# Kernel tuning notes

Measured on AMD Instinct MI355X. Metric: run time of the kernel, lower is better.

Reference implementation:

```python
import jax, jax.numpy as jnp
import numpy as np

ALPHA = 0.2        # LeakyReLU negative slope
NEG_BIG = -9e15    # mask fill value from the original module


def setup_inputs() -> dict:
    key = jax.random.key(0)
    k1, k2, k3, k4 = jax.random.split(key, 4)
    B, N, F_in, F_out = 4, 4096, 128, 64
    h = jax.random.normal(k1, (B, N, F_in), dtype=jnp.float32)
    adj = jax.random.randint(k2, (N, N), 0, 2, dtype=jnp.int32)
    W = jax.random.normal(k3, (F_in, F_out), dtype=jnp.float32)
    a = jax.random.normal(k4, (2 * F_out, 1), dtype=jnp.float32)
    return {"h": h, "adj": adj, "W": W, "a": a}


def reference(h, adj, W, a):
    # h: [B, N, F_in], adj: [N, N], W: [F_in, F_out], a: [2*F_out, 1]
    F_out = W.shape[1]
    hW = jnp.einsum('bni,io->bno', h, W)               # [B, N, F_out]
    f1 = hW @ a[:F_out, :]                             # [B, N, 1]
    f2 = hW @ a[F_out:, :]                             # [B, N, 1]
    e = f1 + jnp.swapaxes(f2, 1, 2)                    # [B, N, N] broadcast-add
    e = jax.nn.leaky_relu(e, negative_slope=ALPHA)
    e = jax.nn.softmax(e, axis=2)
    # dropout is a no-op (is_training=False)
    attention = jnp.where(adj[None, :, :] > 0, e, NEG_BIG)
    new_h = jax.nn.sigmoid(jnp.einsum('bnm,bmo->bno', attention, hW))
    return new_h
```

## Files before the change

kernel.cpp:

```cpp
#include <hip/hip_runtime.h>
#include <hip/hip_bf16.h>


#define GN 4096
#define GB 4
#define FIN 128
#define FOUT 64

typedef int i32x4 __attribute__((ext_vector_type(4)));
typedef unsigned int uint32x4 __attribute__((ext_vector_type(4)));
typedef float f32x4 __attribute__((ext_vector_type(4)));

__global__ __launch_bounds__(1024) void pack_kernel(const int* __restrict__ adj,
                                                    unsigned long long* __restrict__ tmask) {
    __shared__ unsigned short m16[64][68];
    const int t = threadIdx.x;
    const int rt = (int)blockIdx.x >> 2, cp = (int)blockIdx.x & 3;
    const int wrow = t >> 6;
    const int j16 = t & 63;

#pragma unroll
    for (int p = 0; p < 4; ++p) {
        const int row = p * 16 + wrow;
        const i32x4* src = (const i32x4*)(adj + (size_t)(rt * 64 + row) * GN
                                          + cp * 1024 + j16 * 16);
        unsigned int b16 = 0;
#pragma unroll
        for (int q = 0; q < 4; ++q) {
            i32x4 v = src[q];
            b16 |= (v.x == 0 ? 1u : 0u) << (q * 4);
            b16 |= (v.y == 0 ? 2u : 0u) << (q * 4);
            b16 |= (v.z == 0 ? 4u : 0u) << (q * 4);
            b16 |= (v.w == 0 ? 8u : 0u) << (q * 4);
        }
        m16[row][j16] = (unsigned short)b16;
    }
    __syncthreads();

    {
        const int sloc = t >> 6, l = t & 63;
        const int row16 = l & 15, g = l >> 4;
        unsigned long long res = 0ull;
#pragma unroll
        for (int r = 0; r < 4; ++r)
            res |= (unsigned long long)m16[r * 16 + row16][sloc * 4 + g] << (r * 16);
        tmask[((size_t)rt * 64 + cp * 16 + sloc) * 64 + l] = res;
    }
}

__global__ __launch_bounds__(256) void hwrepack_kernel(const float* __restrict__ h,
                                                       const float* __restrict__ W,
                                                       double* __restrict__ hW,
                                                       unsigned char* __restrict__ Bp) {
    __shared__ float Wl[FIN][FOUT];
    const int t = threadIdx.x;
    const int o = t & 63;
    const int a = __builtin_amdgcn_readfirstlane(t >> 6);
    const int bx = (int)blockIdx.x;
    const int b = bx >> 8, rq = bx & 255;

    {
        const f32x4* Wv = (const f32x4*)W;
        f32x4* Wlv = (f32x4*)&Wl[0][0];
#pragma unroll
        for (int c = 0; c < 8; ++c)
            Wlv[c * 256 + t] = Wv[c * 256 + t];
    }
    __syncthreads();

    const int row0 = rq * 16 + a * 4;
    const float* h0 = h + ((size_t)b * GN + row0) * FIN;
    double ac0 = 0, ac1 = 0, ac2 = 0, ac3 = 0;
#pragma unroll 16
    for (int k = 0; k < FIN; ++k) {
        double wd = (double)Wl[k][o];
        ac0 = fma((double)h0[k],           wd, ac0);
        ac1 = fma((double)h0[k + FIN],     wd, ac1);
        ac2 = fma((double)h0[k + 2 * FIN], wd, ac2);
        ac3 = fma((double)h0[k + 3 * FIN], wd, ac3);
    }

    double* hwp = hW + ((size_t)b * GN + row0) * FOUT + o;
    hwp[0]        = ac0;
    hwp[FOUT]     = ac1;
    hwp[2 * FOUT] = ac2;
    hwp[3 * FOUT] = ac3;

    unsigned int w0 = 0, w1 = 0, w2 = 0;
    double accs[4] = {ac0, ac1, ac2, ac3};
#pragma unroll
    for (int rr = 0; rr < 4; ++rr) {
        int qi = (int)llrint(accs[rr] * 65536.0);
        int d0 = ((qi + 128) & 255) - 128; qi = (qi - d0) >> 8;
        int d1 = ((qi + 128) & 255) - 128; qi = (qi - d1) >> 8;
        w0 |= (unsigned int)(d0 & 255) << (rr * 8);
        w1 |= (unsigned int)(d1 & 255) << (rr * 8);
        w2 |= (unsigned int)(qi & 255) << (rr * 8);
    }
    const int q4 = rq * 4 + a;
    const int p = q4 >> 4, g = (q4 >> 2) & 3, qr = q4 & 3;
    const int cg = o >> 4, col16 = o & 15;
    unsigned char* dst = Bp + ((size_t)b * 64 + p) * 12288
                       + cg * 1024 + g * 256 + col16 * 16 + qr * 4;
    *(unsigned int*)(dst)        = w0;
    *(unsigned int*)(dst + 4096) = w1;
    *(unsigned int*)(dst + 8192) = w2;
}

__global__ __launch_bounds__(512, 1) void gemm_kernel(const unsigned char* __restrict__ Bp,
                                                      const unsigned long long* __restrict__ tmask,
                                                      const double* __restrict__ hW,
                                                      float* __restrict__ out) {
    __shared__ __align__(16) unsigned char lds[49152];
    __shared__ unsigned int nflag;
    __shared__ unsigned int flagbuf[128];
    __shared__ double fred[8];

    const int tid = threadIdx.x, lane = tid & 63, wv = tid >> 6;
    const int cg = wv & 3, kg = wv >> 2;
    const int rt = (int)blockIdx.x >> 2, b = (int)blockIdx.x & 3;
    if (tid == 0) nflag = 0;

    const unsigned char* bptr = Bp + (size_t)b * 786432 + kg * 12288 + cg * 1024 + lane * 16;
    const unsigned long long* mptr = tmask + (size_t)rt * 4096 + kg * 64 + lane;

    i32x4 acc[4][3];
#pragma unroll
    for (int r = 0; r < 4; ++r)
#pragma unroll
        for (int pl = 0; pl < 3; ++pl) {
            i32x4 z = {0, 0, 0, 0};
            acc[r][pl] = z;
        }

#define DECLSET(S) i32x4 b##S##0, b##S##1, b##S##2; unsigned long long m##S;
#define LOADSET(S, T) { const unsigned char* g_ = bptr + (size_t)(T) * 24576;          \
        b##S##0 = *(const i32x4*)(g_);                                                 \
        b##S##1 = *(const i32x4*)(g_ + 4096);                                          \
        b##S##2 = *(const i32x4*)(g_ + 8192);                                          \
        m##S = mptr[(size_t)(T) * 128]; }

    DECLSET(A) DECLSET(B) DECLSET(C) DECLSET(D)
    LOADSET(A, 0) LOADSET(B, 1) LOADSET(C, 2) LOADSET(D, 3)

    auto dostep = [&](unsigned long long mw, i32x4 v0, i32x4 v1, i32x4 v2) {
        const unsigned int mlo = (unsigned int)mw, mhi = (unsigned int)(mw >> 32);
#pragma unroll
        for (int r = 0; r < 4; ++r) {
            unsigned int half = (r >> 1) ? mhi : mlo;
            unsigned int w16 = (r & 1) ? (half >> 16) : (half & 0xFFFFu);
            uint32x4 u;
#pragma unroll
            for (int q = 0; q < 4; ++q)
                u[q] = (((w16 >> (4 * q)) & 0xFu) * 0x00204081u) & 0x01010101u;
            i32x4 af = __builtin_bit_cast(i32x4, u);
            acc[r][0] = __builtin_amdgcn_mfma_i32_16x16x64_i8(af, v0, acc[r][0], 0, 0, 0);
            acc[r][1] = __builtin_amdgcn_mfma_i32_16x16x64_i8(af, v1, acc[r][1], 0, 0, 0);
            acc[r][2] = __builtin_amdgcn_mfma_i32_16x16x64_i8(af, v2, acc[r][2], 0, 0, 0);
        }
    };

    for (int T = 0; T < 32; T += 4) {
        dostep(mA, bA0, bA1, bA2);
        if (T + 4 < 32) LOADSET(A, T + 4)
        dostep(mB, bB0, bB1, bB2);
        if (T + 5 < 32) LOADSET(B, T + 5)
        dostep(mC, bC0, bC1, bC2);
        if (T + 6 < 32) LOADSET(C, T + 6)
        dostep(mD, bD0, bD1, bD2);
        if (T + 7 < 32) LOADSET(D, T + 7)
    }
#undef DECLSET
#undef LOADSET

    __syncthreads();
    if (kg == 1) {
        unsigned char* dst = lds + cg * 12288 + lane * 192;
#pragma unroll
        for (int r = 0; r < 4; ++r)
#pragma unroll
            for (int pl = 0; pl < 3; ++pl)
                *(i32x4*)(dst + (r * 3 + pl) * 16) = acc[r][pl];
    }
    __syncthreads();
    if (kg == 0) {
        const unsigned char* s2 = lds + cg * 12288 + lane * 192;
#pragma unroll
        for (int r = 0; r < 4; ++r)
#pragma unroll
            for (int pl = 0; pl < 3; ++pl) {
                i32x4 v = *(const i32x4*)(s2 + (r * 3 + pl) * 16);
#pragma unroll
                for (int q = 0; q < 4; ++q) acc[r][pl][q] += v[q];
            }

        const int o = cg * 16 + (lane & 15);
#pragma unroll
        for (int r = 0; r < 4; ++r) {
#pragma unroll
            for (int q = 0; q < 4; ++q) {
                double S = (double)acc[r][0][q] + 256.0 * (double)acc[r][1][q]
                         + 65536.0 * (double)acc[r][2][q];
                int i = rt * 64 + r * 16 + (lane >> 4) * 4 + q;
                size_t oi = ((size_t)b * GN + i) * FOUT + o;
                out[oi] = S < 0.0 ? 1.0f : 0.0f;
                if (fabs(S) <= 2048.0) {
                    unsigned int idx = atomicAdd(&nflag, 1u);
                    if (idx < 128) flagbuf[idx] = ((unsigned int)i << 6) | (unsigned int)o;
                }
            }
        }
    }

    __syncthreads();
    unsigned int nf = nflag;
    if (nf > 128) nf = 128;
    for (unsigned int f = 0; f < nf; ++f) {
        unsigned int e = flagbuf[f];
        int o = e & 63;
        int i = (int)(e >> 6);
        int row16 = i & 15, r = (i >> 4) & 3;
        int s = tid >> 3, lg = (tid >> 1) & 3, hf = tid & 1;
        unsigned long long w = tmask[((size_t)rt * 64 + s) * 64 + (lg * 16 + row16)];
        double ps = 0.0;
        const double* hwc = hW + ((size_t)b * GN + s * 64 + lg * 16) * FOUT + o;
#pragma unroll
        for (int jj = hf * 8; jj < hf * 8 + 8; ++jj) {
            if ((w >> (r * 16 + jj)) & 1ull)
                ps += hwc[(size_t)jj * FOUT];
        }
#pragma unroll
        for (int d = 32; d >= 1; d >>= 1) ps += __shfl_down(ps, d, 64);
        if (lane == 0) fred[wv] = ps;
        __syncthreads();
        if (tid == 0) {
            double tot = ((fred[0] + fred[1]) + (fred[2] + fred[3]))
                       + ((fred[4] + fred[5]) + (fred[6] + fred[7]));
            out[((size_t)b * GN + i) * FOUT + o] = tot < 0.0 ? 1.0f : 0.0f;
        }
        __syncthreads();
    }
}

extern "C" void kernel_launch(void* const* d_in, const int* in_sizes, int n_in,
                              void* d_out, int out_size, void* d_ws, size_t ws_size,
                              hipStream_t stream) {
    const float* h   = (const float*)d_in[0];
    const int*   adj = (const int*)d_in[1];
    const float* W   = (const float*)d_in[2];
    float* out = (float*)d_out;

    char* ws = (char*)d_ws;
    double* hW                = (double*)ws;
    unsigned char* Bp         = (unsigned char*)(ws + 8388608);
    unsigned long long* tmask = (unsigned long long*)(ws + 12582912);

    pack_kernel<<<256, 1024, 0, stream>>>(adj, tmask);
    hwrepack_kernel<<<1024, 256, 0, stream>>>(h, W, hW, Bp);
    gemm_kernel<<<256, 512, 0, stream>>>(Bp, tmask, hW, out);
}
```

Measured before the change: 55.46 us.

## Compute hW projection with FP64 MFMA from an LDS-staged h tile

Rewrites the h·W projection kernel so each 512-thread block stages a 64-row h tile and W into LDS with coalesced vector loads. The product is then computed with 16x16x4 FP64 MFMA instructions instead of per-thread scalar FP64 FMA loops. Because the MFMA output lane layout is not assumed, each wave checks one scalar reference dot product against candidate layouts and falls back to scalar FMAs if none match. This keeps the fp64 precision the later quantisation relies on, but adds the verification dot product and an LDS transpose buffer, and lowers the block count from 1024 to 256.

```diff
diff --git a/kernel.cpp b/kernel.cpp
--- a/kernel.cpp
+++ b/kernel.cpp
@@ -10,6 +10,7 @@
 typedef int i32x4 __attribute__((ext_vector_type(4)));
 typedef unsigned int uint32x4 __attribute__((ext_vector_type(4)));
 typedef float f32x4 __attribute__((ext_vector_type(4)));
+typedef double f64x4 __attribute__((ext_vector_type(4)));
 
 __global__ __launch_bounds__(1024) void pack_kernel(const int* __restrict__ adj,
                                                     unsigned long long* __restrict__ tmask) {
@@ -36,7 +37,6 @@
         m16[row][j16] = (unsigned short)b16;
     }
     __syncthreads();
-
     {
         const int sloc = t >> 6, l = t & 63;
         const int row16 = l & 15, g = l >> 4;
@@ -48,63 +48,128 @@
     }
 }
 
-__global__ __launch_bounds__(256) void hwrepack_kernel(const float* __restrict__ h,
-                                                       const float* __restrict__ W,
-                                                       double* __restrict__ hW,
-                                                       unsigned char* __restrict__ Bp) {
-    __shared__ float Wl[FIN][FOUT];
+__global__ __launch_bounds__(512, 1) void hwrepack_kernel(const float* __restrict__ h,
+                                                          const float* __restrict__ W,
+                                                          double* __restrict__ hW,
+                                                          unsigned char* __restrict__ Bp) {
+    __shared__ float hs[64][132];
+    __shared__ float Wl[FIN][68];
+    __shared__ double Dt[64][66];
+    __shared__ int smap;
     const int t = threadIdx.x;
-    const int o = t & 63;
-    const int a = __builtin_amdgcn_readfirstlane(t >> 6);
-    const int bx = (int)blockIdx.x;
-    const int b = bx >> 8, rq = bx & 255;
+    const int lane = t & 63, wv = t >> 6;
+    const int bid = (int)blockIdx.x;
 
     {
-        const f32x4* Wv = (const f32x4*)W;
-        f32x4* Wlv = (f32x4*)&Wl[0][0];
-#pragma unroll
-        for (int c = 0; c < 8; ++c)
-            Wlv[c * 256 + t] = Wv[c * 256 + t];
-    }
-    __syncthreads();
-
-    const int row0 = rq * 16 + a * 4;
-    const float* h0 = h + ((size_t)b * GN + row0) * FIN;
-    double ac0 = 0, ac1 = 0, ac2 = 0, ac3 = 0;
-#pragma unroll 16
-    for (int k = 0; k < FIN; ++k) {
-        double wd = (double)Wl[k][o];
-        ac0 = fma((double)h0[k],           wd, ac0);
-        ac1 = fma((double)h0[k + FIN],     wd, ac1);
-        ac2 = fma((double)h0[k + 2 * FIN], wd, ac2);
-        ac3 = fma((double)h0[k + 3 * FIN], wd, ac3);
-    }
-
-    double* hwp = hW + ((size_t)b * GN + row0) * FOUT + o;
-    hwp[0]        = ac0;
-    hwp[FOUT]     = ac1;
-    hwp[2 * FOUT] = ac2;
-    hwp[3 * FOUT] = ac3;
-
-    unsigned int w0 = 0, w1 = 0, w2 = 0;
-    double accs[4] = {ac0, ac1, ac2, ac3};
-#pragma unroll
-    for (int rr = 0; rr < 4; ++rr) {
-        int qi = (int)llrint(accs[rr] * 65536.0);
-        int d0 = ((qi + 128) & 255) - 128; qi = (qi - d0) >> 8;
-        int d1 = ((qi + 128) & 255) - 128; qi = (qi - d1) >> 8;
-        w0 |= (unsigned int)(d0 & 255) << (rr * 8);
-        w1 |= (unsigned int)(d1 & 255) << (rr * 8);
-        w2 |= (unsigned int)(qi & 255) << (rr * 8);
-    }
-    const int q4 = rq * 4 + a;
-    const int p = q4 >> 4, g = (q4 >> 2) & 3, qr = q4 & 3;
-    const int cg = o >> 4, col16 = o & 15;
-    unsigned char* dst = Bp + ((size_t)b * 64 + p) * 12288
-                       + cg * 1024 + g * 256 + col16 * 16 + qr * 4;
-    *(unsigned int*)(dst)        = w0;
-    *(unsigned int*)(dst + 4096) = w1;
-    *(unsigned int*)(dst + 8192) = w2;
+        const f32x4* srcH = (const f32x4*)(h + (size_t)bid * 64 * FIN);
+        const f32x4* srcW = (const f32x4*)W;
+#pragma unroll
+        for (int c = 0; c < 4; ++c) {
+            int idx = c * 512 + t;
+            f32x4 vh = srcH[idx];
+            *(f32x4*)&hs[idx >> 5][(idx & 31) * 4] = vh;
+            f32x4 vw = srcW[idx];
+            *(f32x4*)&Wl[idx >> 4][(idx & 15) * 4] = vw;
+        }
+    }
+    __syncthreads();
+
+    const int mt = wv >> 1, np = wv & 1;
+    const int lr = lane & 15, lk = lane >> 4;
+    f64x4 acc0 = {0.0, 0.0, 0.0, 0.0}, acc1 = {0.0, 0.0, 0.0, 0.0};
+#pragma unroll
+    for (int ks = 0; ks < 32; ++ks) {
+        const int kk = ks * 4 + lk;
+        double A  = (double)hs[mt * 16 + lr][kk];
+        double B0 = (double)Wl[kk][np * 32 + lr];
+        double B1 = (double)Wl[kk][np * 32 + 16 + lr];
+        acc0 = __builtin_amdgcn_mfma_f64_16x16x4f64(A, B0, acc0, 0, 0, 0);
+        acc1 = __builtin_amdgcn_mfma_f64_16x16x4f64(A, B1, acc1, 0, 0, 0);
+    }
+
+    auto dotref = [&](int row, int col) {
+        double s = 0.0;
+#pragma unroll 8
+        for (int k = 0; k < FIN; ++k)
+            s = fma((double)hs[row][k], (double)Wl[k][col], s);
+        return s;
+    };
+    auto allmatch = [&](double ref) {
+        double d = fabs(acc0[0] - ref);
+        int ok = d <= 1e-6 + 1e-6 * fabs(ref);
+        return __ballot(ok) == ~0ull;
+    };
+    int mapid;
+    if      (allmatch(dotref(mt * 16 + 4 * lk, np * 32 + lr))) mapid = 0;
+    else if (allmatch(dotref(mt * 16 + lk,     np * 32 + lr))) mapid = 1;
+    else if (allmatch(dotref(mt * 16 + lr, np * 32 + 4 * lk))) mapid = 2;
+    else if (allmatch(dotref(mt * 16 + lr, np * 32 + lk)))     mapid = 3;
+    else mapid = 4;
+
+    if (mapid != 4) {
+#pragma unroll
+        for (int nt = 0; nt < 2; ++nt) {
+            const f64x4 acv = nt ? acc1 : acc0;
+#pragma unroll
+            for (int q = 0; q < 4; ++q) {
+                int row, col;
+                if (mapid == 0)      { row = mt * 16 + 4 * lk + q; col = np * 32 + nt * 16 + lr; }
+                else if (mapid == 1) { row = mt * 16 + lk + 4 * q; col = np * 32 + nt * 16 + lr; }
+                else if (mapid == 2) { row = mt * 16 + lr; col = np * 32 + nt * 16 + 4 * lk + q; }
+                else                 { row = mt * 16 + lr; col = np * 32 + nt * 16 + lk + 4 * q; }
+                Dt[row][col] = acv[q];
+            }
+        }
+    }
+    if (t == 0) smap = mapid;
+    __syncthreads();
+    const bool fb = (smap == 4);
+
+#pragma unroll
+    for (int u = 0; u < 2; ++u) {
+        const int unit = u * 512 + t;
+        const int col = unit & 63, rg = unit >> 6;
+        double v0, v1, v2, v3;
+        if (fb) {
+            v0 = dotref(rg * 4 + 0, col);
+            v1 = dotref(rg * 4 + 1, col);
+            v2 = dotref(rg * 4 + 2, col);
+            v3 = dotref(rg * 4 + 3, col);
+        } else {
+            v0 = Dt[rg * 4 + 0][col];
+            v1 = Dt[rg * 4 + 1][col];
+            v2 = Dt[rg * 4 + 2][col];
+            v3 = Dt[rg * 4 + 3][col];
+        }
+        const int rowbase = bid * 64 + rg * 4;
+        const int b = rowbase >> 12;
+        const int q4 = (rowbase & 4095) >> 2;
+        const int p = q4 >> 4, g = (q4 >> 2) & 3, qr = q4 & 3;
+
+        double* hwp = hW + (size_t)rowbase * FOUT + col;
+        hwp[0]        = v0;
+        hwp[FOUT]     = v1;
+        hwp[2 * FOUT] = v2;
+        hwp[3 * FOUT] = v3;
+
+        unsigned int w0 = 0, w1 = 0, w2 = 0;
+        double vv[4] = {v0, v1, v2, v3};
+#pragma unroll
+        for (int rr = 0; rr < 4; ++rr) {
+            int qi = (int)llrint(vv[rr] * 65536.0);
+            int d0 = ((qi + 128) & 255) - 128; qi = (qi - d0) >> 8;
+            int d1 = ((qi + 128) & 255) - 128; qi = (qi - d1) >> 8;
+            w0 |= (unsigned int)(d0 & 255) << (rr * 8);
+            w1 |= (unsigned int)(d1 & 255) << (rr * 8);
+            w2 |= (unsigned int)(qi & 255) << (rr * 8);
+        }
+        const int cg = col >> 4, col16 = col & 15;
+        unsigned char* dst = Bp + ((size_t)b * 64 + p) * 12288
+                           + cg * 1024 + g * 256 + col16 * 16 + qr * 4;
+        *(unsigned int*)(dst)        = w0;
+        *(unsigned int*)(dst + 4096) = w1;
+        *(unsigned int*)(dst + 8192) = w2;
+    }
 }
 
 __global__ __launch_bounds__(512, 1) void gemm_kernel(const unsigned char* __restrict__ Bp,
@@ -256,6 +321,6 @@
     unsigned long long* tmask = (unsigned long long*)(ws + 12582912);
 
     pack_kernel<<<256, 1024, 0, stream>>>(adj, tmask);
-    hwrepack_kernel<<<1024, 256, 0, stream>>>(h, W, hW, Bp);
+    hwrepack_kernel<<<256, 512, 0, stream>>>(h, W, hW, Bp);
     gemm_kernel<<<256, 512, 0, stream>>>(Bp, tmask, hW, out);
 }
```

After: 57.41 us. +3.5%, slower.
